# Kernel optimization log

Measured on AMD Instinct MI355X. Metric: run time of the kernel, lower is better.

Reference implementation:

```python
import jax, jax.numpy as jnp
import numpy as np

B, S, E, H = 4, 1024, 1024, 16
HD = E // H  # head_dim = 64
MAX_SEQ = 1024  # rel positions span [-(MAX_SEQ-1), MAX_SEQ-1]


def setup_inputs() -> dict:
    key = jax.random.key(0)
    ks = jax.random.split(key, 12)
    std_e = 1.0 / np.sqrt(E)
    std_h = 1.0 / np.sqrt(HD)
    inp = {
        "x": jax.random.normal(ks[0], (B, S, E), dtype=jnp.float32),
        # torch nn.Linear weights are [out, in]; y = x @ W.T + b
        "Wq": jax.random.uniform(ks[1], (E, E), jnp.float32, -std_e, std_e),
        "bq": jax.random.uniform(ks[2], (E,), jnp.float32, -std_e, std_e),
        "Wk": jax.random.uniform(ks[3], (E, E), jnp.float32, -std_e, std_e),
        "bk": jax.random.uniform(ks[4], (E,), jnp.float32, -std_e, std_e),
        "Wv": jax.random.uniform(ks[5], (E, E), jnp.float32, -std_e, std_e),
        "bv": jax.random.uniform(ks[6], (E,), jnp.float32, -std_e, std_e),
        "Wo": jax.random.uniform(ks[7], (E, E), jnp.float32, -std_e, std_e),
        "bo": jax.random.uniform(ks[8], (E,), jnp.float32, -std_e, std_e),
        # pos_key_proj: Linear(head_dim, head_dim, bias=False)
        "Wp": jax.random.uniform(ks[9], (HD, HD), jnp.float32, -std_h, std_h),
        # learned relative position table [2*max_seq_len-1, head_dim]
        "rel_table": jax.random.normal(ks[10], (2 * MAX_SEQ - 1, HD), dtype=jnp.float32),
    }
    return inp


def _rel_shift(pos_scores):
    # pos_scores: [B, H, S, 2S-1] -> [B, H, S, S]
    # result[..., i, j] = pos_scores[..., i, (S-1) - i + j]
    s = pos_scores.shape[-2]
    idx = (s - 1) - jnp.arange(s)[:, None] + jnp.arange(s)[None, :]  # [S, S]
    return jnp.take_along_axis(pos_scores, idx[None, None, :, :], axis=-1)


def reference(x, Wq, bq, Wk, bk, Wv, bv, Wo, bo, Wp, rel_table):
    scale = 1.0 / np.sqrt(HD)
    Q = (x @ Wq.T + bq).reshape(B, S, H, HD).transpose(0, 2, 1, 3)  # [B,H,S,HD]
    K = (x @ Wk.T + bk).reshape(B, S, H, HD).transpose(0, 2, 1, 3)
    V = (x @ Wv.T + bv).reshape(B, S, H, HD).transpose(0, 2, 1, 3)

    # rel_pos_encoding(S): slice centered at MAX_SEQ-1 covering 2S-1 positions
    center = MAX_SEQ - 1
    rel_emb = rel_table[center - (S - 1): center + S]  # [2S-1, HD]
    rel_key = rel_emb @ Wp.T                            # [2S-1, HD]

    content = jnp.einsum("bhqd,bhkd->bhqk", Q, K) * scale       # [B,H,S,S]
    pos = jnp.einsum("bhqd,pd->bhqp", Q, rel_key) * scale       # [B,H,S,2S-1]
    scores = content + _rel_shift(pos)                          # [B,H,S,S]

    probs = jax.nn.softmax(scores, axis=-1)
    ctx = jnp.einsum("bhqk,bhkd->bhqd", probs, V)               # [B,H,S,HD]
    ctx = ctx.transpose(0, 2, 1, 3).reshape(B, S, E)
    return ctx @ Wo.T + bo
```

## Files before the change

kernel.cpp:

```cpp
#include <hip/hip_runtime.h>
#include <hip/hip_bf16.h>

#define B_   4
#define S_   1024
#define E_   1024
#define H_   16
#define HD_  64

typedef float  f32x4  __attribute__((ext_vector_type(4)));
typedef short  bf16x8 __attribute__((ext_vector_type(8)));
typedef short  bf16x4 __attribute__((ext_vector_type(4)));

__device__ __forceinline__ float bf2f(short u) {
  union { unsigned int i; float f; } v;
  v.i = ((unsigned int)(unsigned short)u) << 16;
  return v.f;
}
__device__ __forceinline__ short f2bf(float f) {
  unsigned int x = __float_as_uint(f);
  x = x + 0x7fffu + ((x >> 16) & 1u);
  return (short)(x >> 16);
}
__device__ __forceinline__ bf16x8 ld_cvt8(const float* __restrict__ p) {
  const f32x4 a = *(const f32x4*)p;
  const f32x4 b = *(const f32x4*)(p + 4);
  bf16x8 r;
  r[0] = f2bf(a[0]); r[1] = f2bf(a[1]); r[2] = f2bf(a[2]); r[3] = f2bf(a[3]);
  r[4] = f2bf(b[0]); r[5] = f2bf(b[1]); r[6] = f2bf(b[2]); r[7] = f2bf(b[3]);
  return r;
}

__device__ __forceinline__ void gload_lds16(const short* g, short* l) {
  __builtin_amdgcn_global_load_lds(
      (const __attribute__((address_space(1))) void*)g,
      (__attribute__((address_space(3))) void*)l, 16, 0, 0);
}

__global__ __launch_bounds__(256) void cvt_f32_bf16(
    const float* __restrict__ src, short* __restrict__ dst, int n)
{
  const int i = (blockIdx.x * 256 + threadIdx.x) * 4;
  if (i < n) {
    const f32x4 v = *(const f32x4*)(src + i);
    bf16x4 o;
    o[0] = f2bf(v[0]); o[1] = f2bf(v[1]); o[2] = f2bf(v[2]); o[3] = f2bf(v[3]);
    *(bf16x4*)(dst + i) = o;
  }
}

__global__ __launch_bounds__(256) void cvt7_f32_bf16(
    const float* __restrict__ w0, const float* __restrict__ w1,
    const float* __restrict__ w2, const float* __restrict__ x,
    short* __restrict__ WB, short* __restrict__ xbf)
{
  const int NW = E_ * E_;
  const int y = blockIdx.y;
  const float* src;
  short* dst;
  if (y < 3) { src = (y == 0) ? w0 : (y == 1) ? w1 : w2; dst = WB + (size_t)y * NW; }
  else       { src = x + (size_t)(y - 3) * NW;           dst = xbf + (size_t)(y - 3) * NW; }
  const int i = (blockIdx.x * 256 + threadIdx.x) * 4;
  const f32x4 v = *(const f32x4*)(src + i);
  bf16x4 o;
  o[0] = f2bf(v[0]); o[1] = f2bf(v[1]); o[2] = f2bf(v[2]); o[3] = f2bf(v[3]);
  *(bf16x4*)(dst + i) = o;
}

template<int TM, int OUTF32>
__global__ __launch_bounds__(256) void gemm_bt(
    const short* __restrict__ A,
    const short* __restrict__ W0, const short* __restrict__ W1, const short* __restrict__ W2,
    const float* __restrict__ b0, const float* __restrict__ b1, const float* __restrict__ b2,
    void* __restrict__ C0v, void* __restrict__ C1v, void* __restrict__ C2v, int vz)
{
  constexpr int NJ = (TM == 128) ? 4 : 2;
  __shared__ short As[TM * 32];
  __shared__ short Bs[128 * 32];

  const int tid  = threadIdx.x;
  const int lane = tid & 63;
  const int wave = tid >> 6;
  const int quad = lane >> 4;
  const int l15  = lane & 15;
  const int wmb  = (TM == 128) ? (wave >> 1) * 64 : 0;
  const int wnb  = (TM == 128) ? (wave & 1) * 64 : wave * 32;
  const int m0   = blockIdx.y * TM;
  const int n0   = blockIdx.x * 128;
  const int z    = blockIdx.z;

  const short* W  = (z == 0) ? W0 : (z == 1) ? W1 : W2;
  const float* bb = (z == 0) ? b0 : (z == 1) ? b1 : b2;
  void*        Cv = (z == 0) ? C0v : (z == 1) ? C1v : C2v;

  const int trow = tid >> 2;
  const int tc   = tid & 3;

  f32x4 acc[4][NJ] = {};

  for (int k0 = 0; k0 < E_; k0 += 32) {
#pragma unroll
    for (int n = 0; n < TM / 64; ++n) {
      const int row  = trow + n * 64;
      const int srcc = tc ^ ((row >> 1) & 3);
      gload_lds16(A + (size_t)(m0 + row) * E_ + k0 + srcc * 8, &As[n * 2048 + tid * 8]);
    }
#pragma unroll
    for (int n = 0; n < 2; ++n) {
      const int row  = trow + n * 64;
      const int srcc = tc ^ ((row >> 1) & 3);
      gload_lds16(W + (size_t)(n0 + row) * E_ + k0 + srcc * 8, &Bs[n * 2048 + tid * 8]);
    }
    __syncthreads();

    bf16x8 af[4], bfr[NJ];
#pragma unroll
    for (int i = 0; i < 4; ++i) {
      const int row = wmb + i * 16 + l15;
      const int pc  = quad ^ ((row >> 1) & 3);
      af[i] = *(bf16x8*)&As[row * 32 + pc * 8];
    }
#pragma unroll
    for (int j = 0; j < NJ; ++j) {
      const int row = wnb + j * 16 + l15;
      const int pc  = quad ^ ((row >> 1) & 3);
      bfr[j] = *(bf16x8*)&Bs[row * 32 + pc * 8];
    }
#pragma unroll
    for (int i = 0; i < 4; ++i)
#pragma unroll
      for (int j = 0; j < NJ; ++j)
        acc[i][j] = __builtin_amdgcn_mfma_f32_16x16x32_bf16(af[i], bfr[j], acc[i][j], 0, 0, 0);
    __syncthreads();
  }

  if (TM == 128 && z == vz) {
    const int mtb = m0 + wmb;
    const int bq  = mtb >> 10;
    const int kt  = (mtb >> 6) & 15;
    short* Cs = (short*)Cv;
#pragma unroll
    for (int j = 0; j < NJ; ++j) {
      const int n = n0 + wnb + j * 16 + l15;
      const float bv = bb[n];
      const int h = (n >> 6) & 15;
      const int d = n & 63;
      bf16x8 lo, hi;
#pragma unroll
      for (int e = 0; e < 8; ++e) {
        lo[e] = f2bf(acc[e & 3][j][e >> 2] + bv);
        hi[e] = f2bf(acc[e & 3][j][(e >> 2) + 2] + bv);
      }
      const size_t off = ((size_t)((bq * 16 + h) * 64 + d)) * 1024 + kt * 64 + quad * 16;
      *(bf16x8*)(Cs + off)     = lo;
      *(bf16x8*)(Cs + off + 8) = hi;
    }
  } else {
#pragma unroll
    for (int j = 0; j < NJ; ++j) {
      const int n = n0 + wnb + j * 16 + l15;
      const float bv = bb[n];
#pragma unroll
      for (int i = 0; i < 4; ++i) {
        const int m = m0 + wmb + i * 16 + quad * 4;
#pragma unroll
        for (int r = 0; r < 4; ++r) {
          const float v = acc[i][j][r] + bv;
          if (OUTF32) ((float*)Cv)[(size_t)(m + r) * E_ + n] = v;
          else        ((short*)Cv)[(size_t)(m + r) * E_ + n] = f2bf(v);
        }
      }
    }
  }
}

__global__ __launch_bounds__(256) void relkey_mfma(
    const float* __restrict__ rel, const float* __restrict__ Wp, short* __restrict__ RKw)
{
  const int tid  = threadIdx.x;
  const int lane = tid & 63;
  const int wv   = tid >> 6;
  const int quad = lane >> 4;
  const int l15  = lane & 15;
  const int p0   = blockIdx.x * 64 + wv * 16;

  bf16x8 af[2];
  {
    int prow = p0 + l15; if (prow > 2046) prow = 2046;
    const float* ap = rel + (size_t)prow * 64 + quad * 8;
    af[0] = ld_cvt8(ap);
    af[1] = ld_cvt8(ap + 32);
  }
  f32x4 acc[4] = {};
#pragma unroll
  for (int nt = 0; nt < 4; ++nt) {
    const float* bp = Wp + (size_t)(nt * 16 + l15) * 64 + quad * 8;
    acc[nt] = __builtin_amdgcn_mfma_f32_16x16x32_bf16(af[0], ld_cvt8(bp),      acc[nt], 0, 0, 0);
    acc[nt] = __builtin_amdgcn_mfma_f32_16x16x32_bf16(af[1], ld_cvt8(bp + 32), acc[nt], 0, 0, 0);
  }
#pragma unroll
  for (int r = 0; r < 4; ++r) {
    const int p = p0 + quad * 4 + r;
    if (p < 2047)
#pragma unroll
      for (int nt = 0; nt < 4; ++nt)
        RKw[(size_t)p * 64 + nt * 16 + l15] = f2bf(acc[nt][r]);
  }
}

__global__ __launch_bounds__(512, 4) void attn_kernel(
    const short* __restrict__ Qw, const short* __restrict__ Kw,
    const short* __restrict__ Vtg, const short* __restrict__ RKw,
    short* __restrict__ Cw)
{
  __shared__ short Ks[64][72];
  __shared__ short Vt[64][72];
  __shared__ short RKs[192][72];
  __shared__ short Ps[8][16][72];

  const int tid  = threadIdx.x;
  const int lane = tid & 63;
  const int wv   = tid >> 6;
  const int quad = lane >> 4;
  const int l15  = lane & 15;
  const int q0   = blockIdx.x * 128;
  const int h    = blockIdx.y;
  const int b    = blockIdx.z;
  const int bh   = b * 16 + h;
  const int qw0  = q0 + wv * 16;
  const int jb   = 112 - 16 * wv;
  const int pbase0 = S_ - 128 - q0;

  bf16x8 qf[2];
  {
    const size_t base = (size_t)(b * S_ + qw0 + l15) * E_ + h * HD_ + quad * 8;
    qf[0] = *(const bf16x8*)(Qw + base);
    qf[1] = *(const bf16x8*)(Qw + base + 32);
  }

  f32x4 oacc[4] = {};
  float lsum[4] = {0.f, 0.f, 0.f, 0.f};

  const float fs = 0.125f * 1.44269504088896340736f;

  const int sr  = tid >> 3;
  const int sc8 = (tid & 7) * 8;

#pragma unroll 1
  for (int kt = 0; kt < 16; ++kt) {
    const int k0 = kt * 64;

    *(bf16x8*)&Ks[sr][sc8] =
        *(const bf16x8*)(Kw + (size_t)(b * S_ + k0 + sr) * E_ + h * HD_ + sc8);
    *(bf16x8*)&Vt[sr][sc8] =
        *(const bf16x8*)(Vtg + (size_t)(bh * 64 + sr) * 1024 + k0 + sc8);
    if (kt == 0) {
#pragma unroll
      for (int jj = 0; jj < 3; ++jj) {
        const int c = tid + jj * 512;
        const int row = c >> 3, ch = (c & 7) * 8;
        int p = pbase0 + row; p = (p > 2046) ? 2046 : p;
        *(bf16x8*)&RKs[row][ch] = *(const bf16x8*)(RKw + (size_t)p * 64 + ch);
      }
    } else {
      const int phys0 = 64 * ((kt + 2) % 3);
      int p = pbase0 + 64 * kt + 128 + sr; p = (p > 2046) ? 2046 : p;
      *(bf16x8*)&RKs[phys0 + sr][sc8] = *(const bf16x8*)(RKw + (size_t)p * 64 + sc8);
    }
    __syncthreads();

    const int s64 = 64 * (kt % 3);

    f32x4 sc[4] = {};
#pragma unroll
    for (int s = 0; s < 2; ++s) {
#pragma unroll
      for (int kk = 0; kk < 4; ++kk) {
        bf16x8 bf = *(bf16x8*)&Ks[kk*16 + l15][s*32 + quad*8];
        sc[kk] = __builtin_amdgcn_mfma_f32_16x16x32_bf16(qf[s], bf, sc[kk], 0, 0, 0);
      }
    }

    f32x4 ta[5] = {};
#pragma unroll
    for (int jt = 0; jt < 5; ++jt) {
      int phys = s64 + jb + jt * 16;
      if (phys >= 192) phys -= 192;
#pragma unroll
      for (int s = 0; s < 2; ++s) {
        bf16x8 bf = *(bf16x8*)&RKs[phys + l15][s*32 + quad*8];
        ta[jt] = __builtin_amdgcn_mfma_f32_16x16x32_bf16(qf[s], bf, ta[jt], 0, 0, 0);
      }
    }

    float p[4][4];
#pragma unroll
    for (int r = 0; r < 4; ++r) {
      const int i16 = quad*4 + r;
      const int d   = 15 + l15 - i16;
      const int srcLane = (quad << 4) | (d & 15);
      float sj[5];
#pragma unroll
      for (int jt = 0; jt < 5; ++jt) sj[jt] = __shfl(ta[jt][r], srcLane, 64);
      const bool hi = (d >= 16);
#pragma unroll
      for (int kk = 0; kk < 4; ++kk) {
        const float t = hi ? sj[kk+1] : sj[kk];
        const float sv = fminf((sc[kk][r] + t) * fs, 108.f);
        const float pv = exp2f(sv - 12.f);
        p[kk][r] = pv;
        lsum[r] += pv;
      }
    }

#pragma unroll
    for (int r = 0; r < 4; ++r) {
      bf16x4 pw;
      pw[0] = f2bf(p[0][r]); pw[1] = f2bf(p[1][r]);
      pw[2] = f2bf(p[2][r]); pw[3] = f2bf(p[3][r]);
      *(bf16x4*)&Ps[wv][quad*4 + r][l15*4] = pw;
    }

#pragma unroll
    for (int ks = 0; ks < 2; ++ks) {
      bf16x8 pa = *(bf16x8*)&Ps[wv][l15][ks*32 + quad*8];
#pragma unroll
      for (int dt = 0; dt < 4; ++dt) {
        bf16x8 vb = *(bf16x8*)&Vt[dt*16 + l15][ks*32 + quad*8];
        oacc[dt] = __builtin_amdgcn_mfma_f32_16x16x32_bf16(pa, vb, oacc[dt], 0, 0, 0);
      }
    }
    __syncthreads();
  }

#pragma unroll
  for (int off = 1; off <= 8; off <<= 1)
#pragma unroll
    for (int r = 0; r < 4; ++r)
      lsum[r] += __shfl_xor(lsum[r], off, 64);

#pragma unroll
  for (int r = 0; r < 4; ++r) {
    const float inv = 1.0f / lsum[r];
    const size_t row = (size_t)(b * S_ + qw0 + quad*4 + r) * E_ + h * HD_;
#pragma unroll
    for (int dt = 0; dt < 4; ++dt)
      Cw[row + dt*16 + l15] = f2bf(oacc[dt][r] * inv);
  }
}

__global__ void fill_kernel(float* __restrict__ out, int n, float val) {
  for (int i = blockIdx.x * blockDim.x + threadIdx.x; i < n; i += gridDim.x * blockDim.x)
    out[i] = val;
}

extern "C" void kernel_launch(void* const* d_in, const int* in_sizes, int n_in,
                              void* d_out, int out_size, void* d_ws, size_t ws_size,
                              hipStream_t stream)
{
  const size_t WS_NEEDED = 33816448;
  if (ws_size < WS_NEEDED) {
    fill_kernel<<<1024, 256, 0, stream>>>((float*)d_out, out_size, 0.25f);
    return;
  }
  if (n_in != 11 || in_sizes[10] != 2047 * 64) {
    fill_kernel<<<1024, 256, 0, stream>>>((float*)d_out, out_size, 0.75f);
    return;
  }

  const float* x   = (const float*)d_in[0];
  const float* Wq  = (const float*)d_in[1];
  const float* bq  = (const float*)d_in[2];
  const float* Wk  = (const float*)d_in[3];
  const float* bk  = (const float*)d_in[4];
  const float* Wv  = (const float*)d_in[5];
  const float* bv  = (const float*)d_in[6];
  const float* Wo  = (const float*)d_in[7];
  const float* bo  = (const float*)d_in[8];
  const float* Wp  = (const float*)d_in[9];
  const float* rel = (const float*)d_in[10];

  char* ws = (char*)d_ws;
  short* Qws = (short*)(ws);
  short* Kws = (short*)(ws + 8388608);
  short* Vtg = (short*)(ws + 16777216);
  short* WB  = (short*)(ws + 25165824);
  short* ctx = (short*)(ws + 25165824);
  short* WoB = (short*)(ws + 8388608);
  short* RKw = (short*)(ws + 33554432);
  short* xbf = (short*)d_out;

  const int NW = E_ * E_;

  cvt7_f32_bf16<<<dim3(1024, 7), dim3(256), 0, stream>>>(Wq, Wk, Wv, x, WB, xbf);

  gemm_bt<128, 0><<<dim3(8, 32, 3), dim3(256), 0, stream>>>(
      xbf, WB, WB + NW, WB + 2 * NW, bq, bk, bv, Qws, Kws, Vtg, 2);

  relkey_mfma<<<dim3(32), dim3(256), 0, stream>>>(rel, Wp, RKw);

  attn_kernel<<<dim3(8, 16, 4), dim3(512), 0, stream>>>(Qws, Kws, Vtg, RKw, ctx);

  cvt_f32_bf16<<<dim3(NW / 1024), dim3(256), 0, stream>>>(Wo, WoB, NW);

  gemm_bt<64, 1><<<dim3(8, 64, 1), dim3(256), 0, stream>>>(
      ctx, WoB, WoB, WoB, bo, bo, bo, d_out, d_out, d_out, -1);
}
```

Baseline: 273.1 us.

## Double-buffer K/V with async LDS loads and stream relative keys from registers

The attention kernel now double-buffers K and V tiles in LDS using direct global-to-LDS loads, issued one tile ahead, with an XOR swizzle in place of padded rows. This leaves one barrier per iteration instead of two. The relative-key ring buffer in LDS is removed, and each lane loads its rel-key fragments straight from global memory into registers. The grid is flattened and remapped so that blocks sharing a (batch, head) pair are spread for better L2 locality, and setprio hints wrap the MFMA sections. The intent is to overlap memory traffic with compute. In exchange it adds more global loads per iteration for the rel keys and relies on correct vmcnt and barrier ordering.

```diff
diff --git a/kernel.cpp b/kernel.cpp
--- a/kernel.cpp
+++ b/kernel.cpp
@@ -212,9 +212,8 @@
     const short* __restrict__ Vtg, const short* __restrict__ RKw,
     short* __restrict__ Cw)
 {
-  __shared__ short Ks[64][72];
-  __shared__ short Vt[64][72];
-  __shared__ short RKs[192][72];
+  __shared__ short Ks[2][64][64];
+  __shared__ short Vt[2][64][64];
   __shared__ short Ps[8][16][72];
 
   const int tid  = threadIdx.x;
@@ -222,10 +221,13 @@
   const int wv   = tid >> 6;
   const int quad = lane >> 4;
   const int l15  = lane & 15;
-  const int q0   = blockIdx.x * 128;
-  const int h    = blockIdx.y;
-  const int b    = blockIdx.z;
-  const int bh   = b * 16 + h;
+
+  const int lid  = blockIdx.x;
+  const int pair = (lid & 7) * 8 + ((lid >> 3) >> 3);
+  const int qt   = (lid >> 3) & 7;
+  const int b    = pair >> 4;
+  const int h    = pair & 15;
+  const int q0   = qt * 128;
   const int qw0  = q0 + wv * 16;
   const int jb   = 112 - 16 * wv;
   const int pbase0 = S_ - 128 - q0;
@@ -237,65 +239,74 @@
     qf[1] = *(const bf16x8*)(Qw + base + 32);
   }
 
+  const int sr  = tid >> 3;
+  const int ssw = (tid & 7) ^ (sr & 7);
+  const short* Ksrc0 = Kw  + (size_t)(b * S_ + sr) * E_ + h * HD_ + ssw * 8;
+  const short* Vsrc0 = Vtg + (size_t)(pair * 64 + sr) * 1024 + ssw * 8;
+  short* Kdst = &Ks[0][0][0] + (size_t)tid * 8;
+  short* Vdst = &Vt[0][0][0] + (size_t)tid * 8;
+
+  gload_lds16(Ksrc0, Kdst);
+  gload_lds16(Vsrc0, Vdst);
+
   f32x4 oacc[4] = {};
   float lsum[4] = {0.f, 0.f, 0.f, 0.f};
-
   const float fs = 0.125f * 1.44269504088896340736f;
-
-  const int sr  = tid >> 3;
-  const int sc8 = (tid & 7) * 8;
+  const int swz = l15 & 7;
 
 #pragma unroll 1
   for (int kt = 0; kt < 16; ++kt) {
-    const int k0 = kt * 64;
-
-    *(bf16x8*)&Ks[sr][sc8] =
-        *(const bf16x8*)(Kw + (size_t)(b * S_ + k0 + sr) * E_ + h * HD_ + sc8);
-    *(bf16x8*)&Vt[sr][sc8] =
-        *(const bf16x8*)(Vtg + (size_t)(bh * 64 + sr) * 1024 + k0 + sc8);
-    if (kt == 0) {
-#pragma unroll
-      for (int jj = 0; jj < 3; ++jj) {
-        const int c = tid + jj * 512;
-        const int row = c >> 3, ch = (c & 7) * 8;
-        int p = pbase0 + row; p = (p > 2046) ? 2046 : p;
-        *(bf16x8*)&RKs[row][ch] = *(const bf16x8*)(RKw + (size_t)p * 64 + ch);
-      }
-    } else {
-      const int phys0 = 64 * ((kt + 2) % 3);
-      int p = pbase0 + 64 * kt + 128 + sr; p = (p > 2046) ? 2046 : p;
-      *(bf16x8*)&RKs[phys0 + sr][sc8] = *(const bf16x8*)(RKw + (size_t)p * 64 + sc8);
-    }
-    __syncthreads();
-
-    const int s64 = 64 * (kt % 3);
-
-    f32x4 sc[4] = {};
-#pragma unroll
-    for (int s = 0; s < 2; ++s) {
+    const int cur = kt & 1;
+
+    __builtin_amdgcn_sched_barrier(0);
+    asm volatile("s_waitcnt vmcnt(0)" ::: "memory");
+    __builtin_amdgcn_s_barrier();
+    __builtin_amdgcn_sched_barrier(0);
+
+    bf16x8 rkb[5][2];
+    {
+      const int pb = pbase0 + 64 * kt + jb + l15;
+#pragma unroll
+      for (int jt = 0; jt < 5; ++jt) {
+        int p = pb + jt * 16; if (p > 2046) p = 2046;
+        const short* rp = RKw + (size_t)p * 64 + quad * 8;
+        rkb[jt][0] = *(const bf16x8*)rp;
+        rkb[jt][1] = *(const bf16x8*)(rp + 32);
+      }
+    }
+
+    if (kt < 15) {
+      const int nb = (kt + 1) & 1;
+      gload_lds16(Ksrc0 + (size_t)(kt + 1) * 64 * E_, Kdst + nb * 4096);
+      gload_lds16(Vsrc0 + (kt + 1) * 64,              Vdst + nb * 4096);
+    }
+    __builtin_amdgcn_sched_barrier(0);
+
+    f32x4 sc4[4] = {};
+    __builtin_amdgcn_s_setprio(1);
+#pragma unroll
+    for (int s = 0; s < 2; ++s)
 #pragma unroll
       for (int kk = 0; kk < 4; ++kk) {
-        bf16x8 bf = *(bf16x8*)&Ks[kk*16 + l15][s*32 + quad*8];
-        sc[kk] = __builtin_amdgcn_mfma_f32_16x16x32_bf16(qf[s], bf, sc[kk], 0, 0, 0);
-      }
-    }
+        const int pc = (s * 4 + quad) ^ swz;
+        bf16x8 bf = *(bf16x8*)&Ks[cur][kk * 16 + l15][pc * 8];
+        sc4[kk] = __builtin_amdgcn_mfma_f32_16x16x32_bf16(qf[s], bf, sc4[kk], 0, 0, 0);
+      }
+    __builtin_amdgcn_s_setprio(0);
 
     f32x4 ta[5] = {};
+    __builtin_amdgcn_s_setprio(1);
 #pragma unroll
     for (int jt = 0; jt < 5; ++jt) {
-      int phys = s64 + jb + jt * 16;
-      if (phys >= 192) phys -= 192;
-#pragma unroll
-      for (int s = 0; s < 2; ++s) {
-        bf16x8 bf = *(bf16x8*)&RKs[phys + l15][s*32 + quad*8];
-        ta[jt] = __builtin_amdgcn_mfma_f32_16x16x32_bf16(qf[s], bf, ta[jt], 0, 0, 0);
-      }
-    }
+      ta[jt] = __builtin_amdgcn_mfma_f32_16x16x32_bf16(qf[0], rkb[jt][0], ta[jt], 0, 0, 0);
+      ta[jt] = __builtin_amdgcn_mfma_f32_16x16x32_bf16(qf[1], rkb[jt][1], ta[jt], 0, 0, 0);
+    }
+    __builtin_amdgcn_s_setprio(0);
 
     float p[4][4];
 #pragma unroll
     for (int r = 0; r < 4; ++r) {
-      const int i16 = quad*4 + r;
+      const int i16 = quad * 4 + r;
       const int d   = 15 + l15 - i16;
       const int srcLane = (quad << 4) | (d & 15);
       float sj[5];
@@ -304,8 +315,8 @@
       const bool hi = (d >= 16);
 #pragma unroll
       for (int kk = 0; kk < 4; ++kk) {
-        const float t = hi ? sj[kk+1] : sj[kk];
-        const float sv = fminf((sc[kk][r] + t) * fs, 108.f);
+        const float t = hi ? sj[kk + 1] : sj[kk];
+        const float sv = fminf((sc4[kk][r] + t) * fs, 108.f);
         const float pv = exp2f(sv - 12.f);
         p[kk][r] = pv;
         lsum[r] += pv;
@@ -317,19 +328,21 @@
       bf16x4 pw;
       pw[0] = f2bf(p[0][r]); pw[1] = f2bf(p[1][r]);
       pw[2] = f2bf(p[2][r]); pw[3] = f2bf(p[3][r]);
-      *(bf16x4*)&Ps[wv][quad*4 + r][l15*4] = pw;
-    }
-
+      *(bf16x4*)&Ps[wv][quad * 4 + r][l15 * 4] = pw;
+    }
+
+    __builtin_amdgcn_s_setprio(1);
 #pragma unroll
     for (int ks = 0; ks < 2; ++ks) {
-      bf16x8 pa = *(bf16x8*)&Ps[wv][l15][ks*32 + quad*8];
+      bf16x8 pa = *(bf16x8*)&Ps[wv][l15][ks * 32 + quad * 8];
 #pragma unroll
       for (int dt = 0; dt < 4; ++dt) {
-        bf16x8 vb = *(bf16x8*)&Vt[dt*16 + l15][ks*32 + quad*8];
+        const int pc = (ks * 4 + quad) ^ swz;
+        bf16x8 vb = *(bf16x8*)&Vt[cur][dt * 16 + l15][pc * 8];
         oacc[dt] = __builtin_amdgcn_mfma_f32_16x16x32_bf16(pa, vb, oacc[dt], 0, 0, 0);
       }
     }
-    __syncthreads();
+    __builtin_amdgcn_s_setprio(0);
   }
 
 #pragma unroll
@@ -341,10 +354,10 @@
 #pragma unroll
   for (int r = 0; r < 4; ++r) {
     const float inv = 1.0f / lsum[r];
-    const size_t row = (size_t)(b * S_ + qw0 + quad*4 + r) * E_ + h * HD_;
+    const size_t row = (size_t)(b * S_ + qw0 + quad * 4 + r) * E_ + h * HD_;
 #pragma unroll
     for (int dt = 0; dt < 4; ++dt)
-      Cw[row + dt*16 + l15] = f2bf(oacc[dt][r] * inv);
+      Cw[row + dt * 16 + l15] = f2bf(oacc[dt][r] * inv);
   }
 }
 
@@ -398,7 +411,7 @@
 
   relkey_mfma<<<dim3(32), dim3(256), 0, stream>>>(rel, Wp, RKw);
 
-  attn_kernel<<<dim3(8, 16, 4), dim3(512), 0, stream>>>(Qws, Kws, Vtg, RKw, ctx);
+  attn_kernel<<<dim3(512), dim3(512), 0, stream>>>(Qws, Kws, Vtg, RKw, ctx);
 
   cvt_f32_bf16<<<dim3(NW / 1024), dim3(256), 0, stream>>>(Wo, WoB, NW);
 
```

Result: slower. 302.8 us (+10.8%).
